# Performance work log

Hardware: AMD Instinct MI355X
Metric: run time of the kernel (lower is better)

The kernel has to match this reference:

```python
import jax, jax.numpy as jnp
import numpy as np

SELF_DIM = 6   # self_state_dim
HID = 50       # lstm_hidden_dim


def setup_inputs() -> dict:
    key = jax.random.key(0)
    ks = jax.random.split(key, 16)
    B, N, D = 8192, 64, 13  # batch, num humans, joint-state length

    def w(k, shape):
        # kaiming-ish init, stored as [in, out] so forward is x @ W + b
        return jax.random.normal(k, shape, jnp.float32) / jnp.sqrt(jnp.float32(shape[0]))

    z = lambda n: jnp.zeros((n,), jnp.float32)
    return {
        "state": jax.random.normal(ks[0], (B, N, D), jnp.float32),
        # mlp1: 13 -> 150 -> 100, last_relu=True
        "mlp1_w1": w(ks[1], (13, 150)),  "mlp1_b1": z(150),
        "mlp1_w2": w(ks[2], (150, 100)), "mlp1_b2": z(100),
        # attention: 200 -> 100 -> 100 -> 1 (no relu on last)
        "attn_w1": w(ks[3], (200, 100)), "attn_b1": z(100),
        "attn_w2": w(ks[4], (100, 100)), "attn_b2": z(100),
        "attn_w3": w(ks[5], (100, 1)),   "attn_b3": z(1),
        # LSTM(input=7, hidden=50), torch gate order i,f,g,o
        "lstm_wih": w(ks[6], (7, 4 * HID)),
        "lstm_whh": w(ks[7], (HID, 4 * HID)),
        "lstm_bih": z(4 * HID), "lstm_bhh": z(4 * HID),
        # mlp: 56 -> 150 -> 100 -> 100 -> 1
        "mlp_w1": w(ks[8], (SELF_DIM + HID, 150)), "mlp_b1": z(150),
        "mlp_w2": w(ks[9], (150, 100)),            "mlp_b2": z(100),
        "mlp_w3": w(ks[10], (100, 100)),           "mlp_b3": z(100),
        "mlp_w4": w(ks[11], (100, 1)),             "mlp_b4": z(1),
    }


def reference(state, mlp1_w1, mlp1_b1, mlp1_w2, mlp1_b2,
              attn_w1, attn_b1, attn_w2, attn_b2, attn_w3, attn_b3,
              lstm_wih, lstm_whh, lstm_bih, lstm_bhh,
              mlp_w1, mlp_b1, mlp_w2, mlp_b2, mlp_w3, mlp_b3, mlp_w4, mlp_b4):
    relu = jax.nn.relu
    B, N, D = state.shape
    self_state = state[:, 0, :SELF_DIM]      # [B, 6]
    human_state = state[:, :, SELF_DIM:]     # [B, N, 7]

    # mlp1 over all B*N per-human joint-state rows (last_relu=True)
    flat = state.reshape(B * N, D)
    m1 = relu(relu(flat @ mlp1_w1 + mlp1_b1) @ mlp1_w2 + mlp1_b2)   # [B*N, 100]

    # mean-pooled global state, broadcast back per human, concat, attention score
    gdim = m1.shape[-1]
    global_state = jnp.mean(m1.reshape(B, N, gdim), axis=1, keepdims=True)
    global_state = jnp.broadcast_to(global_state, (B, N, gdim)).reshape(B * N, gdim)
    a_in = jnp.concatenate([m1, global_state], axis=1)               # [B*N, 200]
    scores = (relu(relu(a_in @ attn_w1 + attn_b1) @ attn_w2 + attn_b2) @ attn_w3 + attn_b3)
    scores = scores.reshape(B, N)
    # NOTE: in the original torch code `scores` only feed `rerank_human_state`,
    # which is never consumed (dead code) -- the LSTM runs on the UNSORTED
    # human_state. We keep the score computation for fidelity; the per-sample
    # argsort/gather is dropped since it does not affect the output.

    # LSTM over the N humans (batch_first in torch, h0=c0=0)
    xs = jnp.transpose(human_state, (1, 0, 2))   # [N, B, 7]
    h0 = jnp.zeros((B, HID), state.dtype)

    def step(carry, x_t):
        h, c = carry
        gates = x_t @ lstm_wih + h @ lstm_whh + lstm_bih + lstm_bhh  # [B, 4H]
        i, f, g, o = jnp.split(gates, 4, axis=-1)
        c = jax.nn.sigmoid(f) * c + jax.nn.sigmoid(i) * jnp.tanh(g)
        h = jax.nn.sigmoid(o) * jnp.tanh(c)
        return (h, c), None

    (hn, _cn), _ = jax.lax.scan(step, (h0, h0), xs)

    # value head on [self_state, h_n]
    joint = jnp.concatenate([self_state, hn], axis=1)   # [B, 56]
    x = relu(joint @ mlp_w1 + mlp_b1)
    x = relu(x @ mlp_w2 + mlp_b2)
    x = relu(x @ mlp_w3 + mlp_b3)
    value = x @ mlp_w4 + mlp_b4                          # [B, 1]
    return value
```

## Files before the change

kernel.cpp:

```cpp
#include <hip/hip_runtime.h>

typedef __attribute__((ext_vector_type(8))) short short8;
typedef __attribute__((ext_vector_type(4))) float f32x4;
union frag_u { short8 v; unsigned short u[8]; };

__device__ __forceinline__ float bf2f(unsigned short b) {
  unsigned int u = ((unsigned int)b) << 16;
  float f; __builtin_memcpy(&f, &u, 4); return f;
}
__device__ __forceinline__ unsigned short f2bf(float f) {
  unsigned int u; __builtin_memcpy(&u, &f, 4);
  return (unsigned short)((u + 0x7FFFu + ((u >> 16) & 1u)) >> 16);
}
__device__ __forceinline__ unsigned short hi_of(float f) { return f2bf(f); }
__device__ __forceinline__ unsigned short lo_of(float f) {
  unsigned short h = f2bf(f); return f2bf(f - bf2f(h));
}

__device__ __forceinline__ void lstm_act(float gi, float gf, float gg, float go,
                                         float& c, float& h) {
  gi = fminf(fmaxf(gi, -15.f), 15.f);
  gf = fminf(fmaxf(gf, -15.f), 15.f);
  gg = fminf(fmaxf(gg, -15.f), 15.f);
  go = fminf(fmaxf(go, -15.f), 15.f);
  float A = 1.f + __expf(-gf);
  float B = 1.f + __expf(-gi);
  float C = 1.f + __expf(2.f * gg);
  float BC  = B * C;
  float num = c * BC + A * (C - 2.f);
  c = num * __builtin_amdgcn_rcpf(A * BC);
  float D  = 1.f + __expf(-go);
  float cl = fminf(fmaxf(c, -15.f), 15.f);
  float E  = 1.f + __expf(2.f * cl);
  h = (E - 2.f) * __builtin_amdgcn_rcpf(D * E);
}

__global__ void detect_dtype_kernel(const unsigned short* s, int* flag) {
  int i = threadIdx.x;
  unsigned short v = s[2 * i];
  int e = (v >> 7) & 0xFF;
  unsigned long long m = __ballot(e < 100 || e > 140);
  if (i == 0) *flag = (__popcll(m) >= 16) ? 1 : 0;
}

template <int AS, typename GetB, typename GetW>
__device__ __forceinline__ void mfma_layer(const unsigned short* sA, float* sG,
    int wave, int col, int quad, int kc_n, int ntiles, int N, GetB getb, GetW getw)
{
  for (int tile = wave; tile < ntiles; tile += 16) {
    int n = tile * 16 + col;
    float b = (n < N) ? getb(n) : 0.f;
    f32x4 acc = {b, b, b, b};
    for (int kc = 0; kc < kc_n; ++kc) {
      short8 a = *(const short8*)&sA[col * AS + kc * 32 + quad * 8];
      frag_u w;
      #pragma unroll
      for (int j = 0; j < 8; ++j) {
        int k = kc * 32 + quad * 8 + j;
        w.u[j] = (n < N) ? getw(k, n) : (unsigned short)0;
      }
      acc = __builtin_amdgcn_mfma_f32_16x16x32_bf16(a, w.v, acc, 0, 0, 0);
    }
    *(f32x4*)&sG[n * 20 + quad * 4] = acc;
  }
}

template <int AS, bool LO>
__device__ __forceinline__ void relu_fill(const float* sG, unsigned short* sA,
                                          int tid, int N, int loOff, int Kpad) {
  for (int idx = tid; idx < 16 * Kpad; idx += 1024) {
    int m = idx & 15, n = idx >> 4;
    unsigned short v = 0;
    if (n < N) {
      v = f2bf(fmaxf(sG[n * 20 + m], 0.f));
    } else if (LO && n >= loOff && n < loOff + N) {
      float x = fmaxf(sG[(n - loOff) * 20 + m], 0.f);
      v = lo_of(x);
    }
    sA[m * AS + n] = v;
  }
}

template <bool F32>
__global__ __launch_bounds__(1024, 8) void value_net_kernel(
    const void* state_, const void* wih_, const void* whh_,
    const void* bih_, const void* bhh_,
    const void* w1_, const void* b1_, const void* w2_, const void* b2_,
    const void* w3_, const void* b3_, const void* w4_, const void* b4_,
    void* out_, const int* flag)
{
  if (flag && *flag != (F32 ? 1 : 0)) return;

  constexpr int AS = F32 ? 328 : 168;
  constexpr int KC = F32 ? 6 : 4;

  __shared__ __align__(16) unsigned short sA[2][16 * AS];
  __shared__ __align__(16) float sG[208 * 20];
  __shared__ __align__(16) unsigned short sX[1024 * 8 * (F32 ? 2 : 1)];

  const unsigned short* st16 = (const unsigned short*)state_;
  const float*          stf  = (const float*)state_;

  const int tid  = threadIdx.x;
  const int wave = tid >> 6;
  const int lane = tid & 63;
  const int col  = lane & 15;
  const int quad = lane >> 4;
  const int r0   = blockIdx.x * 16;

  {
    unsigned int* a32 = (unsigned int*)&sA[0][0];
    constexpr int ZT = 16 * AS;
    #pragma unroll
    for (int i = 0; i < (ZT + 1023) / 1024; ++i) {
      int idx = tid + i * 1024;
      if (idx < ZT) a32[idx] = 0;
    }
  }

  {
    int r = tid >> 6, t = tid & 63;
    size_t g = (size_t)(r0 + r) * 832 + (size_t)t * 13 + 6;
    int base = (t * 16 + r) * 8;
    if constexpr (!F32) {
      #pragma unroll
      for (int d = 0; d < 7; ++d) sX[base + d] = st16[g + d];
    } else {
      #pragma unroll
      for (int d = 0; d < 7; ++d) {
        float f = stf[g + d];
        unsigned short h = f2bf(f);
        sX[2 * (base + d) + 0] = h;
        sX[2 * (base + d) + 1] = f2bf(f - bf2f(h));
      }
    }
  }

  auto W_lstm = [&](int k, int n) -> unsigned short {
    if constexpr (!F32) {
      const unsigned short* wih = (const unsigned short*)wih_;
      const unsigned short* whh = (const unsigned short*)whh_;
      if (k < 7)   return wih[k * 200 + n];
      if (k < 8)   return (unsigned short)0;
      if (k < 108) return whh[((k - 8) >> 1) * 200 + n];
      return (unsigned short)0;
    } else {
      const float* wih = (const float*)wih_;
      const float* whh = (const float*)whh_;
      if (k < 7)   return hi_of(wih[k * 200 + n]);
      if (k < 14)  return hi_of(wih[(k - 7) * 200 + n]);
      if (k < 21)  return lo_of(wih[(k - 14) * 200 + n]);
      if (k < 22)  return (unsigned short)0;
      if (k < 122) return hi_of(whh[((k - 22) >> 1) * 200 + n]);
      if (k < 172) return lo_of(whh[(k - 122) * 200 + n]);
      return (unsigned short)0;
    }
  };
  auto ldf = [&](const void* p, int i) -> float {
    if constexpr (F32) return ((const float*)p)[i];
    else               return bf2f(((const unsigned short*)p)[i]);
  };

  const bool hasTile = (wave < 13);
  frag_u wf[KC];
  float  wb = 0.f;
  if (hasTile) {
    int nn = wave * 16 + col;
    int no = (nn < 200) ? ((nn & 3) * 50 + (nn >> 2)) : 0;
    #pragma unroll
    for (int kc = 0; kc < KC; ++kc) {
      #pragma unroll
      for (int j = 0; j < 8; ++j) {
        int k = kc * 32 + quad * 8 + j;
        wf[kc].u[j] = (nn < 200) ? W_lstm(k, no) : (unsigned short)0;
      }
    }
    wb = (nn < 200) ? (ldf(bih_, no) + ldf(bhh_, no)) : 0.f;
  }

  const int  u_   = wave * 4 + quad;
  const bool iact = hasTile && (u_ < 50);
  float c_ = 0.f, hf = 0.f;

  const bool isx = (tid >= 832) && (tid < 944);
  const int  xm = (tid - 832) / 7, xd = (tid - 832) - ((tid - 832) / 7) * 7;
  auto xfeed = [&](unsigned short* sAw, int t) {
    int base = (t * 16 + xm) * 8 + xd;
    if constexpr (!F32) {
      sAw[xm * AS + xd] = sX[base];
    } else {
      unsigned short h = sX[2 * base + 0], l = sX[2 * base + 1];
      sAw[xm * AS + xd] = h; sAw[xm * AS + 14 + xd] = h;
      sAw[xm * AS + 7 + xd] = l;
    }
  };

  __syncthreads();
  if (isx) xfeed(&sA[0][0], 0);
  __syncthreads();

  for (int t = 0; t < 64; ++t) {
    const unsigned short* sAr = &sA[t & 1][0];
    unsigned short*       sAw = &sA[(t & 1) ^ 1][0];

    if (hasTile) {
      short8 a[KC];
      #pragma unroll
      for (int kc = 0; kc < KC; ++kc)
        a[kc] = *(const short8*)&sAr[col * AS + kc * 32 + quad * 8];
      f32x4 acc = {wb, wb, wb, wb};
      #pragma unroll
      for (int kc = 0; kc < KC; ++kc)
        acc = __builtin_amdgcn_mfma_f32_16x16x32_bf16(a[kc], wf[kc].v, acc, 0, 0, 0);
      *(f32x4*)&sG[(wave * 16 + col) * 20 + quad * 4] = acc;

      if (iact) {
        int nb = wave * 16 + quad * 4;
        float gi = sG[(nb + 0) * 20 + col];
        float gf = sG[(nb + 1) * 20 + col];
        float gg = sG[(nb + 2) * 20 + col];
        float go = sG[(nb + 3) * 20 + col];
        float h;
        lstm_act(gi, gf, gg, go, c_, h);
        if (t < 63) {
          unsigned short hb = f2bf(h);
          unsigned short hl = f2bf(h - bf2f(hb));
          unsigned int pack = (unsigned int)hb | ((unsigned int)hl << 16);
          if constexpr (!F32) {
            *(unsigned int*)&sAw[col * AS + 8 + 2 * u_] = pack;
          } else {
            *(unsigned int*)&sAw[col * AS + 22 + 2 * u_] = pack;
            sAw[col * AS + 122 + u_] = hb;
          }
        } else hf = h;
      }
    } else if (isx && t < 63) {
      xfeed(sAw, t + 1);
    }
    __syncthreads();
  }

  unsigned short* sA0 = &sA[0][0];
  {
    unsigned int* a32 = (unsigned int*)sA0;
    #pragma unroll
    for (int i = 0; i < (16 * AS / 2 + 1023) / 1024; ++i) {
      int idx = tid + i * 1024;
      if (idx < 16 * AS / 2) a32[idx] = 0;
    }
  }
  __syncthreads();
  if (iact) {
    unsigned short hb = f2bf(hf);
    unsigned short hl = f2bf(hf - bf2f(hb));
    sA0[col * AS + 6 + u_] = hb;
    if constexpr (!F32) sA0[col * AS + 56 + u_] = hl; else sA0[col * AS + 62 + u_] = hl;
  }
  if (tid < 96) {
    int m = tid / 6, d = tid - (tid / 6) * 6;
    if constexpr (!F32) sA0[m * AS + d] = st16[(size_t)(r0 + m) * 832 + d];
    else {
      float f = stf[(size_t)(r0 + m) * 832 + d];
      sA0[m * AS + d] = hi_of(f); sA0[m * AS + 56 + d] = lo_of(f);
    }
  }
  __syncthreads();

  mfma_layer<AS>(sA0, sG, wave, col, quad, 4, 10, 150,
    [&](int n) { return ldf(b1_, n); },
    [&](int k, int n) -> unsigned short {
      if constexpr (!F32) {
        const unsigned short* w1 = (const unsigned short*)w1_;
        if (k < 56)  return w1[k * 150 + n];
        if (k < 106) return w1[(k - 50) * 150 + n];
        return (unsigned short)0;
      } else {
        const float* w1 = (const float*)w1_;
        if (k < 56)  return hi_of(w1[k * 150 + n]);
        if (k < 112) return hi_of(w1[(k - 56) * 150 + n]);
        return (unsigned short)0;
      }
    });
  __syncthreads();
  if constexpr (!F32) relu_fill<AS, false>(sG, sA0, tid, 150, 160, 160);
  else                relu_fill<AS, true >(sG, sA0, tid, 150, 150, 320);
  __syncthreads();

  mfma_layer<AS>(sA0, sG, wave, col, quad, F32 ? 10 : 5, 7, 100,
    [&](int n) { return ldf(b2_, n); },
    [&](int k, int n) -> unsigned short {
      if constexpr (!F32) {
        const unsigned short* w2 = (const unsigned short*)w2_;
        return (k < 150) ? w2[k * 100 + n] : (unsigned short)0;
      } else {
        const float* w2 = (const float*)w2_;
        if (k < 150) return hi_of(w2[k * 100 + n]);
        if (k < 300) return hi_of(w2[(k - 150) * 100 + n]);
        return (unsigned short)0;
      }
    });
  __syncthreads();
  if constexpr (!F32) relu_fill<AS, false>(sG, sA0, tid, 100, 128, 128);
  else                relu_fill<AS, true >(sG, sA0, tid, 100, 100, 224);
  __syncthreads();

  mfma_layer<AS>(sA0, sG, wave, col, quad, F32 ? 7 : 4, 7, 100,
    [&](int n) { return ldf(b3_, n); },
    [&](int k, int n) -> unsigned short {
      if constexpr (!F32) {
        const unsigned short* w3 = (const unsigned short*)w3_;
        return (k < 100) ? w3[k * 100 + n] : (unsigned short)0;
      } else {
        const float* w3 = (const float*)w3_;
        if (k < 100) return hi_of(w3[k * 100 + n]);
        if (k < 200) return hi_of(w3[(k - 100) * 100 + n]);
        return (unsigned short)0;
      }
    });
  __syncthreads();

  if (tid < 256) {
    int m = tid >> 4, j0 = tid & 15;
    float s = 0.f;
    for (int j = j0; j < 100; j += 16)
      s += fmaxf(sG[j * 20 + m], 0.f) * ldf(w4_, j);
    s += __shfl_xor(s, 8); s += __shfl_xor(s, 4);
    s += __shfl_xor(s, 2); s += __shfl_xor(s, 1);
    if (j0 == 0) {
      float v = s + ldf(b4_, 0);
      if constexpr (!F32) ((unsigned short*)out_)[r0 + m] = f2bf(v);
      else                ((float*)out_)[r0 + m] = v;
    }
  }
}

extern "C" void kernel_launch(void* const* d_in, const int* in_sizes, int n_in,
                              void* d_out, int out_size, void* d_ws, size_t ws_size,
                              hipStream_t stream) {
  (void)n_in; (void)out_size;
  const void* state = d_in[0];
  const void* wih = d_in[11]; const void* whh = d_in[12];
  const void* bih = d_in[13]; const void* bhh = d_in[14];
  const void* w1  = d_in[15]; const void* b1  = d_in[16];
  const void* w2  = d_in[17]; const void* b2  = d_in[18];
  const void* w3  = d_in[19]; const void* b3  = d_in[20];
  const void* w4  = d_in[21]; const void* b4  = d_in[22];

  const long long F32B  = 8192LL * 64 * 13 * 4;
  const long long BF16B = 8192LL * 64 * 13 * 2;
  long long sz = in_sizes ? (long long)in_sizes[0] : -1;

  if (sz == F32B) {
    value_net_kernel<true><<<dim3(512), dim3(1024), 0, stream>>>(
        state, wih, whh, bih, bhh, w1, b1, w2, b2, w3, b3, w4, b4, d_out,
        (const int*)nullptr);
  } else if (sz == BF16B) {
    value_net_kernel<false><<<dim3(512), dim3(1024), 0, stream>>>(
        state, wih, whh, bih, bhh, w1, b1, w2, b2, w3, b3, w4, b4, d_out,
        (const int*)nullptr);
  } else if (ws_size >= sizeof(int)) {
    int* flag = (int*)d_ws;
    detect_dtype_kernel<<<dim3(1), dim3(64), 0, stream>>>(
        (const unsigned short*)state, flag);
    value_net_kernel<false><<<dim3(512), dim3(1024), 0, stream>>>(
        state, wih, whh, bih, bhh, w1, b1, w2, b2, w3, b3, w4, b4, d_out, flag);
    value_net_kernel<true><<<dim3(512), dim3(1024), 0, stream>>>(
        state, wih, whh, bih, bhh, w1, b1, w2, b2, w3, b3, w4, b4, d_out, flag);
  } else {
    value_net_kernel<false><<<dim3(512), dim3(1024), 0, stream>>>(
        state, wih, whh, bih, bhh, w1, b1, w2, b2, w3, b3, w4, b4, d_out,
        (const int*)nullptr);
  }
}
```

Measured before the change: 235.5 us.

## Restructure LSTM into 4-wave blocks with register-held hidden state and swapped MFMA operands

Shrinks each block from 16 waves to 4. Each wave computes 3-4 gate tiles with the weights as the MFMA A operand, so the four gates of a hidden unit land in one lane's accumulator and no longer go through shared memory. The hidden state is kept packed (bf16 hi/lo) in registers and exchanged between waves through a small double-buffered shared array, with one barrier per step. The input x and the bias are folded into the first K chunk, with the bias taken as a constant-1 column. This cuts per-step barrier and LDS traffic in the serial recurrence, in exchange for complex index mapping and heavy register use (24 weight fragments per lane). The bf16 path now also uses the hi/lo split layout, so it does more MFMA work.

```diff
diff --git a/kernel.cpp b/kernel.cpp
--- a/kernel.cpp
+++ b/kernel.cpp
@@ -2,7 +2,8 @@
 
 typedef __attribute__((ext_vector_type(8))) short short8;
 typedef __attribute__((ext_vector_type(4))) float f32x4;
-union frag_u { short8 v; unsigned short u[8]; };
+typedef __attribute__((ext_vector_type(4))) unsigned int u32x4;
+union frag_u { short8 v; unsigned short u[8]; unsigned int w[4]; };
 
 __device__ __forceinline__ float bf2f(unsigned short b) {
   unsigned int u = ((unsigned int)b) << 16;
@@ -16,6 +17,8 @@
 __device__ __forceinline__ unsigned short lo_of(float f) {
   unsigned short h = f2bf(f); return f2bf(f - bf2f(h));
 }
+__device__ __forceinline__ float ldf_f32(const void* p, int i) { return ((const float*)p)[i]; }
+__device__ __forceinline__ float ldf_b16(const void* p, int i) { return bf2f(((const unsigned short*)p)[i]); }
 
 __device__ __forceinline__ void lstm_act(float gi, float gf, float gg, float go,
                                          float& c, float& h) {
@@ -26,12 +29,12 @@
   float A = 1.f + __expf(-gf);
   float B = 1.f + __expf(-gi);
   float C = 1.f + __expf(2.f * gg);
-  float BC  = B * C;
+  float BC = B * C;
   float num = c * BC + A * (C - 2.f);
   c = num * __builtin_amdgcn_rcpf(A * BC);
-  float D  = 1.f + __expf(-go);
+  float D = 1.f + __expf(-go);
   float cl = fminf(fmaxf(c, -15.f), 15.f);
-  float E  = 1.f + __expf(2.f * cl);
+  float E = 1.f + __expf(2.f * cl);
   h = (E - 2.f) * __builtin_amdgcn_rcpf(D * E);
 }
 
@@ -43,13 +46,61 @@
   if (i == 0) *flag = (__popcll(m) >= 16) ? 1 : 0;
 }
 
+template <bool F32>
+__device__ __forceinline__ unsigned short W_elem(
+    int k, int T, int nl,
+    const void* wih_, const void* whh_, const void* bih_, const void* bhh_) {
+  const int O[4] = {1, 2, 3, 0};
+  int qd = nl >> 2, g = nl & 3;
+  int uc = 4 * T + O[qd];
+  if (uc >= 50) return 0;
+  int no = g * 50 + uc;
+  auto whi = [&](const void* p, int idx) -> unsigned short {
+    if constexpr (F32) return hi_of(((const float*)p)[idx]);
+    else return ((const unsigned short*)p)[idx];
+  };
+  auto wlo = [&](const void* p, int idx) -> unsigned short {
+    if constexpr (F32) return lo_of(((const float*)p)[idx]);
+    else return 0;
+  };
+  if (k < 21) {
+    int d = k / 3, sl = k - 3 * d;
+    return (sl == 2) ? wlo(wih_, d * 200 + no) : whi(wih_, d * 200 + no);
+  }
+  if (k < 23) {
+    float b;
+    if constexpr (F32) b = ((const float*)bih_)[no] + ((const float*)bhh_)[no];
+    else b = bf2f(((const unsigned short*)bih_)[no]) + bf2f(((const unsigned short*)bhh_)[no]);
+    if (k == 21) return f2bf(b);
+    unsigned short bh = f2bf(b);
+    return f2bf(b - bf2f(bh));
+  }
+  if (k < 24) return 0;
+  if (k < 128) {
+    int idx = k - 24, wA = idx >> 3, s = (idx & 7) >> 1;
+    int qB = (3 + wA) & 3, t = 4 * (wA >> 2) + s;
+    if (t > ((qB == 3) ? 12 : 11)) return 0;
+    int u = 4 * t + O[qB];
+    if (u >= 50) return 0;
+    return whi(whh_, u * 200 + no);
+  }
+  int idx = k - 128, wB = idx >> 3, j7 = idx & 7;
+  int qB = wB & 3, t = 8 * (wB >> 2) + j7;
+  if (wB == 4 && j7 >= 5)
+    return (j7 <= 6) ? whi(whh_, 49 * 200 + no) : 0;
+  if (t > ((qB == 0 || qB == 3) ? 12 : 11)) return 0;
+  int u = 4 * t + O[qB];
+  if (u >= 50) return 0;
+  return wlo(whh_, u * 200 + no);
+}
+
 template <int AS, typename GetB, typename GetW>
 __device__ __forceinline__ void mfma_layer(const unsigned short* sA, float* sG,
     int wave, int col, int quad, int kc_n, int ntiles, int N, GetB getb, GetW getw)
 {
-  for (int tile = wave; tile < ntiles; tile += 16) {
-    int n = tile * 16 + col;
-    float b = (n < N) ? getb(n) : 0.f;
+  for (int tile = wave; tile < ntiles; tile += 4) {
+    int nn = tile * 16 + col;
+    float b = (nn < N) ? getb(nn) : 0.f;
     f32x4 acc = {b, b, b, b};
     for (int kc = 0; kc < kc_n; ++kc) {
       short8 a = *(const short8*)&sA[col * AS + kc * 32 + quad * 8];
@@ -57,32 +108,32 @@
       #pragma unroll
       for (int j = 0; j < 8; ++j) {
         int k = kc * 32 + quad * 8 + j;
-        w.u[j] = (n < N) ? getw(k, n) : (unsigned short)0;
+        w.u[j] = (nn < N) ? getw(k, nn) : (unsigned short)0;
       }
       acc = __builtin_amdgcn_mfma_f32_16x16x32_bf16(a, w.v, acc, 0, 0, 0);
     }
-    *(f32x4*)&sG[n * 20 + quad * 4] = acc;
-  }
-}
-
-template <int AS, bool LO>
+    *(f32x4*)&sG[nn * 20 + quad * 4] = acc;
+  }
+}
+
+template <int AS>
 __device__ __forceinline__ void relu_fill(const float* sG, unsigned short* sA,
                                           int tid, int N, int loOff, int Kpad) {
-  for (int idx = tid; idx < 16 * Kpad; idx += 1024) {
-    int m = idx & 15, n = idx >> 4;
+  for (int idx = tid; idx < 16 * Kpad; idx += 256) {
+    int m = idx & 15, nn = idx >> 4;
     unsigned short v = 0;
-    if (n < N) {
-      v = f2bf(fmaxf(sG[n * 20 + m], 0.f));
-    } else if (LO && n >= loOff && n < loOff + N) {
-      float x = fmaxf(sG[(n - loOff) * 20 + m], 0.f);
+    if (nn < N) {
+      v = f2bf(fmaxf(sG[nn * 20 + m], 0.f));
+    } else if (nn >= loOff && nn < loOff + N) {
+      float x = fmaxf(sG[(nn - loOff) * 20 + m], 0.f);
       v = lo_of(x);
     }
-    sA[m * AS + n] = v;
+    sA[m * AS + nn] = v;
   }
 }
 
 template <bool F32>
-__global__ __launch_bounds__(1024, 8) void value_net_kernel(
+__global__ __launch_bounds__(256, 2) void value_net_kernel(
     const void* state_, const void* wih_, const void* whh_,
     const void* bih_, const void* bhh_,
     const void* w1_, const void* b1_, const void* w2_, const void* b2_,
@@ -91,242 +142,242 @@
 {
   if (flag && *flag != (F32 ? 1 : 0)) return;
 
-  constexpr int AS = F32 ? 328 : 168;
-  constexpr int KC = F32 ? 6 : 4;
-
-  __shared__ __align__(16) unsigned short sA[2][16 * AS];
+  constexpr int AS = 328;
+
+  __shared__ __align__(16) unsigned int sX[1024 * 8];
+  __shared__ unsigned int sE[2][13 * 64];
+  __shared__ __align__(16) unsigned short sA[16 * AS];
   __shared__ __align__(16) float sG[208 * 20];
-  __shared__ __align__(16) unsigned short sX[1024 * 8 * (F32 ? 2 : 1)];
 
   const unsigned short* st16 = (const unsigned short*)state_;
   const float*          stf  = (const float*)state_;
 
   const int tid  = threadIdx.x;
-  const int wave = tid >> 6;
+  const int wv   = tid >> 6;
   const int lane = tid & 63;
-  const int col  = lane & 15;
+  const int n    = lane & 15;
   const int quad = lane >> 4;
   const int r0   = blockIdx.x * 16;
 
-  {
-    unsigned int* a32 = (unsigned int*)&sA[0][0];
-    constexpr int ZT = 16 * AS;
+  const int O[4] = {1, 2, 3, 0};
+  const int ores = O[quad];
+  const int tb   = (wv == 0) ? 0 : (wv == 1) ? 4 : (wv == 2) ? 7 : 10;
+  const int nt   = (wv == 0) ? 4 : 3;
+
+  auto ldf = [&](const void* p, int i) -> float {
+    if constexpr (F32) return ldf_f32(p, i); else return ldf_b16(p, i);
+  };
+
+  for (int idx = tid; idx < 1024; idx += 256) {
+    int t = idx >> 4, r = idx & 15;
+    size_t g = (size_t)(r0 + r) * 832 + (size_t)t * 13 + 6;
+    unsigned int* dst = &sX[(t * 16 + r) * 8];
     #pragma unroll
-    for (int i = 0; i < (ZT + 1023) / 1024; ++i) {
-      int idx = tid + i * 1024;
-      if (idx < ZT) a32[idx] = 0;
-    }
-  }
-
-  {
-    int r = tid >> 6, t = tid & 63;
-    size_t g = (size_t)(r0 + r) * 832 + (size_t)t * 13 + 6;
-    int base = (t * 16 + r) * 8;
-    if constexpr (!F32) {
-      #pragma unroll
-      for (int d = 0; d < 7; ++d) sX[base + d] = st16[g + d];
-    } else {
-      #pragma unroll
-      for (int d = 0; d < 7; ++d) {
+    for (int d = 0; d < 7; ++d) {
+      unsigned int v;
+      if constexpr (F32) {
         float f = stf[g + d];
         unsigned short h = f2bf(f);
-        sX[2 * (base + d) + 0] = h;
-        sX[2 * (base + d) + 1] = f2bf(f - bf2f(h));
+        v = (unsigned int)h | ((unsigned int)f2bf(f - bf2f(h)) << 16);
+      } else v = st16[g + d];
+      dst[d] = v;
+    }
+    dst[7] = 0;
+  }
+
+  frag_u wf[4][6];
+  #pragma unroll
+  for (int Ti = 0; Ti < 4; ++Ti) {
+    if (Ti < nt) {
+      int T = tb + Ti;
+      #pragma unroll
+      for (int kc = 0; kc < 6; ++kc)
+        #pragma unroll
+        for (int j = 0; j < 8; ++j)
+          wf[Ti][kc].u[j] = W_elem<F32>(kc * 32 + quad * 8 + j, T, n,
+                                        wih_, whh_, bih_, bhh_);
+    }
+  }
+
+  unsigned int pk[16];
+  #pragma unroll
+  for (int i = 0; i < 16; ++i) pk[i] = 0;
+  float c_[4] = {0.f, 0.f, 0.f, 0.f};
+
+  __syncthreads();
+
+  auto hh = [](unsigned int a, unsigned int b) -> unsigned int {
+    return (a & 0xffffu) | (b << 16);
+  };
+  auto ror16 = [](unsigned int a) -> unsigned int {
+    return (a >> 16) | (a << 16);
+  };
+  auto packh = [](float h) -> unsigned int {
+    unsigned short hb = f2bf(h);
+    unsigned short hl = f2bf(h - bf2f(hb));
+    return (unsigned int)hb | ((unsigned int)hl << 16);
+  };
+
+  #pragma unroll 1
+  for (int tt = 0; tt < 64; ++tt) {
+    const u32x4* xp = (const u32x4*)&sX[(tt * 16 + n) * 8];
+    u32x4 xa = xp[0], xb = xp[1];
+    unsigned int px0 = xa[0], px1 = xa[1], px2 = xa[2], px3 = xa[3];
+    unsigned int px4 = xb[0], px5 = xb[1], px6 = xb[2];
+    const unsigned int ONE = 0x3F80u;
+
+    frag_u fr0, fr1, fr2, fr3, fr4, fr5;
+    if (quad == 0) {
+      fr0.w[0] = px0; fr0.w[1] = hh(px0, px1); fr0.w[2] = ror16(px1); fr0.w[3] = px2;
+    } else if (quad == 1) {
+      fr0.w[0] = hh(px2, px3); fr0.w[1] = ror16(px3); fr0.w[2] = px4; fr0.w[3] = hh(px4, px5);
+    } else if (quad == 2) {
+      fr0.w[0] = ror16(px5); fr0.w[1] = px6; fr0.w[2] = hh(px6, ONE); fr0.w[3] = ONE;
+    } else {
+      fr0.w[0] = pk[0]; fr0.w[1] = pk[1]; fr0.w[2] = pk[2]; fr0.w[3] = pk[3];
+    }
+    bool q3 = (quad == 3);
+    fr1.w[0] = q3 ? pk[4]  : pk[0];  fr1.w[1] = q3 ? pk[5]  : pk[1];
+    fr1.w[2] = q3 ? pk[6]  : pk[2];  fr1.w[3] = q3 ? pk[7]  : pk[3];
+    fr2.w[0] = q3 ? pk[8]  : pk[4];  fr2.w[1] = q3 ? pk[9]  : pk[5];
+    fr2.w[2] = q3 ? pk[10] : pk[6];  fr2.w[3] = q3 ? pk[11] : pk[7];
+    fr3.w[0] = q3 ? pk[12] : pk[8];  fr3.w[1] = q3 ? 0u     : pk[9];
+    fr3.w[2] = q3 ? 0u     : pk[10]; fr3.w[3] = q3 ? 0u     : pk[11];
+    fr4.w[0] = hh(pk[0], pk[1]); fr4.w[1] = hh(pk[2], pk[3]);
+    fr4.w[2] = hh(pk[4], pk[5]); fr4.w[3] = hh(pk[6], pk[7]);
+    fr5.w[0] = hh(pk[8], pk[9]); fr5.w[1] = hh(pk[10], pk[11]);
+    if (quad == 0) { fr5.w[2] = hh(pk[12], pk[12]); fr5.w[3] = pk[12] >> 16; }
+    else           { fr5.w[2] = hh(pk[12], 0u);     fr5.w[3] = 0u; }
+
+    f32x4 z = {0.f, 0.f, 0.f, 0.f};
+    f32x4 acc0 = z, acc1 = z, acc2 = z, acc3 = z;
+    #pragma unroll
+    for (int kc = 0; kc < 6; ++kc) {
+      const frag_u& fr = (kc == 0) ? fr0 : (kc == 1) ? fr1 : (kc == 2) ? fr2 :
+                         (kc == 3) ? fr3 : (kc == 4) ? fr4 : fr5;
+      acc0 = __builtin_amdgcn_mfma_f32_16x16x32_bf16(wf[0][kc].v, fr.v, acc0, 0, 0, 0);
+      acc1 = __builtin_amdgcn_mfma_f32_16x16x32_bf16(wf[1][kc].v, fr.v, acc1, 0, 0, 0);
+      acc2 = __builtin_amdgcn_mfma_f32_16x16x32_bf16(wf[2][kc].v, fr.v, acc2, 0, 0, 0);
+      if (wv == 0)
+        acc3 = __builtin_amdgcn_mfma_f32_16x16x32_bf16(wf[3][kc].v, fr.v, acc3, 0, 0, 0);
+    }
+
+    unsigned int pknew0 = 0, pknew1 = 0, pknew2 = 0, pknew3 = 0;
+    { int u = 4 * (tb + 0) + ores;
+      if (u < 50) { float h; lstm_act(acc0[0], acc0[1], acc0[2], acc0[3], c_[0], h); pknew0 = packh(h); } }
+    { int u = 4 * (tb + 1) + ores;
+      if (u < 50) { float h; lstm_act(acc1[0], acc1[1], acc1[2], acc1[3], c_[1], h); pknew1 = packh(h); } }
+    { int u = 4 * (tb + 2) + ores;
+      if (u < 50) { float h; lstm_act(acc2[0], acc2[1], acc2[2], acc2[3], c_[2], h); pknew2 = packh(h); } }
+    if (wv == 0) { float h; lstm_act(acc3[0], acc3[1], acc3[2], acc3[3], c_[3], h); pknew3 = packh(h); }
+
+    if (tt < 63) {
+      unsigned int* e = sE[tt & 1];
+      if      (wv == 0) { e[0 + lane] = pknew0; e[64 + lane] = pknew1; e[128 + lane] = pknew2; e[192 + lane] = pknew3; }
+      else if (wv == 1) { e[256 + lane] = pknew0; e[320 + lane] = pknew1; e[384 + lane] = pknew2; }
+      else if (wv == 2) { e[448 + lane] = pknew0; e[512 + lane] = pknew1; e[576 + lane] = pknew2; }
+      else              { e[640 + lane] = pknew0; e[704 + lane] = pknew1; e[768 + lane] = pknew2; }
+    }
+    if      (wv == 0) { pk[0] = pknew0; pk[1] = pknew1; pk[2] = pknew2; pk[3] = pknew3; }
+    else if (wv == 1) { pk[4] = pknew0; pk[5] = pknew1; pk[6] = pknew2; }
+    else if (wv == 2) { pk[7] = pknew0; pk[8] = pknew1; pk[9] = pknew2; }
+    else              { pk[10] = pknew0; pk[11] = pknew1; pk[12] = pknew2; }
+    if (tt < 63) {
+      __syncthreads();
+      const unsigned int* e = sE[tt & 1];
+      if (wv == 0) {
+        pk[4] = e[256 + lane]; pk[5] = e[320 + lane]; pk[6] = e[384 + lane];
+        pk[7] = e[448 + lane]; pk[8] = e[512 + lane]; pk[9] = e[576 + lane];
+        pk[10] = e[640 + lane]; pk[11] = e[704 + lane]; pk[12] = e[768 + lane];
+      } else if (wv == 1) {
+        pk[0] = e[0 + lane]; pk[1] = e[64 + lane]; pk[2] = e[128 + lane]; pk[3] = e[192 + lane];
+        pk[7] = e[448 + lane]; pk[8] = e[512 + lane]; pk[9] = e[576 + lane];
+        pk[10] = e[640 + lane]; pk[11] = e[704 + lane]; pk[12] = e[768 + lane];
+      } else if (wv == 2) {
+        pk[0] = e[0 + lane]; pk[1] = e[64 + lane]; pk[2] = e[128 + lane]; pk[3] = e[192 + lane];
+        pk[4] = e[256 + lane]; pk[5] = e[320 + lane]; pk[6] = e[384 + lane];
+        pk[10] = e[640 + lane]; pk[11] = e[704 + lane]; pk[12] = e[768 + lane];
+      } else {
+        pk[0] = e[0 + lane]; pk[1] = e[64 + lane]; pk[2] = e[128 + lane]; pk[3] = e[192 + lane];
+        pk[4] = e[256 + lane]; pk[5] = e[320 + lane]; pk[6] = e[384 + lane];
+        pk[7] = e[448 + lane]; pk[8] = e[512 + lane]; pk[9] = e[576 + lane];
       }
     }
   }
 
-  auto W_lstm = [&](int k, int n) -> unsigned short {
-    if constexpr (!F32) {
-      const unsigned short* wih = (const unsigned short*)wih_;
-      const unsigned short* whh = (const unsigned short*)whh_;
-      if (k < 7)   return wih[k * 200 + n];
-      if (k < 8)   return (unsigned short)0;
-      if (k < 108) return whh[((k - 8) >> 1) * 200 + n];
-      return (unsigned short)0;
-    } else {
-      const float* wih = (const float*)wih_;
-      const float* whh = (const float*)whh_;
-      if (k < 7)   return hi_of(wih[k * 200 + n]);
-      if (k < 14)  return hi_of(wih[(k - 7) * 200 + n]);
-      if (k < 21)  return lo_of(wih[(k - 14) * 200 + n]);
-      if (k < 22)  return (unsigned short)0;
-      if (k < 122) return hi_of(whh[((k - 22) >> 1) * 200 + n]);
-      if (k < 172) return lo_of(whh[(k - 122) * 200 + n]);
-      return (unsigned short)0;
-    }
-  };
-  auto ldf = [&](const void* p, int i) -> float {
-    if constexpr (F32) return ((const float*)p)[i];
-    else               return bf2f(((const unsigned short*)p)[i]);
-  };
-
-  const bool hasTile = (wave < 13);
-  frag_u wf[KC];
-  float  wb = 0.f;
-  if (hasTile) {
-    int nn = wave * 16 + col;
-    int no = (nn < 200) ? ((nn & 3) * 50 + (nn >> 2)) : 0;
-    #pragma unroll
-    for (int kc = 0; kc < KC; ++kc) {
-      #pragma unroll
-      for (int j = 0; j < 8; ++j) {
-        int k = kc * 32 + quad * 8 + j;
-        wf[kc].u[j] = (nn < 200) ? W_lstm(k, no) : (unsigned short)0;
+  {
+    unsigned int* a32 = (unsigned int*)sA;
+    for (int idx = tid; idx < 16 * AS / 2; idx += 256) a32[idx] = 0;
+  }
+  __syncthreads();
+  {
+    auto jput = [&](int t, unsigned int p) {
+      int u = 4 * t + ores;
+      if (u < 50) {
+        sA[n * AS + 6 + u]  = (unsigned short)(p & 0xffffu);
+        sA[n * AS + 62 + u] = (unsigned short)(p >> 16);
       }
-    }
-    wb = (nn < 200) ? (ldf(bih_, no) + ldf(bhh_, no)) : 0.f;
-  }
-
-  const int  u_   = wave * 4 + quad;
-  const bool iact = hasTile && (u_ < 50);
-  float c_ = 0.f, hf = 0.f;
-
-  const bool isx = (tid >= 832) && (tid < 944);
-  const int  xm = (tid - 832) / 7, xd = (tid - 832) - ((tid - 832) / 7) * 7;
-  auto xfeed = [&](unsigned short* sAw, int t) {
-    int base = (t * 16 + xm) * 8 + xd;
-    if constexpr (!F32) {
-      sAw[xm * AS + xd] = sX[base];
-    } else {
-      unsigned short h = sX[2 * base + 0], l = sX[2 * base + 1];
-      sAw[xm * AS + xd] = h; sAw[xm * AS + 14 + xd] = h;
-      sAw[xm * AS + 7 + xd] = l;
-    }
-  };
-
-  __syncthreads();
-  if (isx) xfeed(&sA[0][0], 0);
-  __syncthreads();
-
-  for (int t = 0; t < 64; ++t) {
-    const unsigned short* sAr = &sA[t & 1][0];
-    unsigned short*       sAw = &sA[(t & 1) ^ 1][0];
-
-    if (hasTile) {
-      short8 a[KC];
-      #pragma unroll
-      for (int kc = 0; kc < KC; ++kc)
-        a[kc] = *(const short8*)&sAr[col * AS + kc * 32 + quad * 8];
-      f32x4 acc = {wb, wb, wb, wb};
-      #pragma unroll
-      for (int kc = 0; kc < KC; ++kc)
-        acc = __builtin_amdgcn_mfma_f32_16x16x32_bf16(a[kc], wf[kc].v, acc, 0, 0, 0);
-      *(f32x4*)&sG[(wave * 16 + col) * 20 + quad * 4] = acc;
-
-      if (iact) {
-        int nb = wave * 16 + quad * 4;
-        float gi = sG[(nb + 0) * 20 + col];
-        float gf = sG[(nb + 1) * 20 + col];
-        float gg = sG[(nb + 2) * 20 + col];
-        float go = sG[(nb + 3) * 20 + col];
-        float h;
-        lstm_act(gi, gf, gg, go, c_, h);
-        if (t < 63) {
-          unsigned short hb = f2bf(h);
-          unsigned short hl = f2bf(h - bf2f(hb));
-          unsigned int pack = (unsigned int)hb | ((unsigned int)hl << 16);
-          if constexpr (!F32) {
-            *(unsigned int*)&sAw[col * AS + 8 + 2 * u_] = pack;
-          } else {
-            *(unsigned int*)&sAw[col * AS + 22 + 2 * u_] = pack;
-            sAw[col * AS + 122 + u_] = hb;
-          }
-        } else hf = h;
-      }
-    } else if (isx && t < 63) {
-      xfeed(sAw, t + 1);
-    }
-    __syncthreads();
-  }
-
-  unsigned short* sA0 = &sA[0][0];
-  {
-    unsigned int* a32 = (unsigned int*)sA0;
-    #pragma unroll
-    for (int i = 0; i < (16 * AS / 2 + 1023) / 1024; ++i) {
-      int idx = tid + i * 1024;
-      if (idx < 16 * AS / 2) a32[idx] = 0;
-    }
-  }
-  __syncthreads();
-  if (iact) {
-    unsigned short hb = f2bf(hf);
-    unsigned short hl = f2bf(hf - bf2f(hb));
-    sA0[col * AS + 6 + u_] = hb;
-    if constexpr (!F32) sA0[col * AS + 56 + u_] = hl; else sA0[col * AS + 62 + u_] = hl;
+    };
+    if      (wv == 0) { jput(0, pk[0]); jput(1, pk[1]); jput(2, pk[2]); jput(3, pk[3]); }
+    else if (wv == 1) { jput(4, pk[4]); jput(5, pk[5]); jput(6, pk[6]); }
+    else if (wv == 2) { jput(7, pk[7]); jput(8, pk[8]); jput(9, pk[9]); }
+    else              { jput(10, pk[10]); jput(11, pk[11]); jput(12, pk[12]); }
   }
   if (tid < 96) {
     int m = tid / 6, d = tid - (tid / 6) * 6;
-    if constexpr (!F32) sA0[m * AS + d] = st16[(size_t)(r0 + m) * 832 + d];
-    else {
+    if constexpr (F32) {
       float f = stf[(size_t)(r0 + m) * 832 + d];
-      sA0[m * AS + d] = hi_of(f); sA0[m * AS + 56 + d] = lo_of(f);
-    }
-  }
-  __syncthreads();
-
-  mfma_layer<AS>(sA0, sG, wave, col, quad, 4, 10, 150,
-    [&](int n) { return ldf(b1_, n); },
-    [&](int k, int n) -> unsigned short {
-      if constexpr (!F32) {
-        const unsigned short* w1 = (const unsigned short*)w1_;
-        if (k < 56)  return w1[k * 150 + n];
-        if (k < 106) return w1[(k - 50) * 150 + n];
-        return (unsigned short)0;
-      } else {
-        const float* w1 = (const float*)w1_;
-        if (k < 56)  return hi_of(w1[k * 150 + n]);
-        if (k < 112) return hi_of(w1[(k - 56) * 150 + n]);
-        return (unsigned short)0;
-      }
+      sA[m * AS + d] = hi_of(f); sA[m * AS + 56 + d] = lo_of(f);
+    } else {
+      sA[m * AS + d] = st16[(size_t)(r0 + m) * 832 + d];
+    }
+  }
+  __syncthreads();
+
+  auto whiT = [&](const void* p, int idx) -> unsigned short {
+    if constexpr (F32) return hi_of(((const float*)p)[idx]);
+    else return ((const unsigned short*)p)[idx];
+  };
+
+  mfma_layer<AS>(sA, sG, wv, n, quad, 4, 10, 150,
+    [&](int nn) { return ldf(b1_, nn); },
+    [&](int k, int nn) -> unsigned short {
+      if (k < 56)  return whiT(w1_, k * 150 + nn);
+      if (k < 112) return whiT(w1_, (k - 56) * 150 + nn);
+      return (unsigned short)0;
     });
   __syncthreads();
-  if constexpr (!F32) relu_fill<AS, false>(sG, sA0, tid, 150, 160, 160);
-  else                relu_fill<AS, true >(sG, sA0, tid, 150, 150, 320);
-  __syncthreads();
-
-  mfma_layer<AS>(sA0, sG, wave, col, quad, F32 ? 10 : 5, 7, 100,
-    [&](int n) { return ldf(b2_, n); },
-    [&](int k, int n) -> unsigned short {
-      if constexpr (!F32) {
-        const unsigned short* w2 = (const unsigned short*)w2_;
-        return (k < 150) ? w2[k * 100 + n] : (unsigned short)0;
-      } else {
-        const float* w2 = (const float*)w2_;
-        if (k < 150) return hi_of(w2[k * 100 + n]);
-        if (k < 300) return hi_of(w2[(k - 150) * 100 + n]);
-        return (unsigned short)0;
-      }
+  relu_fill<AS>(sG, sA, tid, 150, 150, 320);
+  __syncthreads();
+
+  mfma_layer<AS>(sA, sG, wv, n, quad, 10, 7, 100,
+    [&](int nn) { return ldf(b2_, nn); },
+    [&](int k, int nn) -> unsigned short {
+      if (k < 150) return whiT(w2_, k * 100 + nn);
+      if (k < 300) return whiT(w2_, (k - 150) * 100 + nn);
+      return (unsigned short)0;
     });
   __syncthreads();
-  if constexpr (!F32) relu_fill<AS, false>(sG, sA0, tid, 100, 128, 128);
-  else                relu_fill<AS, true >(sG, sA0, tid, 100, 100, 224);
-  __syncthreads();
-
-  mfma_layer<AS>(sA0, sG, wave, col, quad, F32 ? 7 : 4, 7, 100,
-    [&](int n) { return ldf(b3_, n); },
-    [&](int k, int n) -> unsigned short {
-      if constexpr (!F32) {
-        const unsigned short* w3 = (const unsigned short*)w3_;
-        return (k < 100) ? w3[k * 100 + n] : (unsigned short)0;
-      } else {
-        const float* w3 = (const float*)w3_;
-        if (k < 100) return hi_of(w3[k * 100 + n]);
-        if (k < 200) return hi_of(w3[(k - 100) * 100 + n]);
-        return (unsigned short)0;
-      }
+  relu_fill<AS>(sG, sA, tid, 100, 100, 224);
+  __syncthreads();
+
+  mfma_layer<AS>(sA, sG, wv, n, quad, 7, 7, 100,
+    [&](int nn) { return ldf(b3_, nn); },
+    [&](int k, int nn) -> unsigned short {
+      if (k < 100) return whiT(w3_, k * 100 + nn);
+      if (k < 200) return whiT(w3_, (k - 100) * 100 + nn);
+      return (unsigned short)0;
     });
   __syncthreads();
 
-  if (tid < 256) {
-    int m = tid >> 4, j0 = tid & 15;
+  if (tid < 64) {
+    int m = lane & 15, j0 = lane >> 4;
     float s = 0.f;
-    for (int j = j0; j < 100; j += 16)
+    for (int j = j0; j < 100; j += 4)
       s += fmaxf(sG[j * 20 + m], 0.f) * ldf(w4_, j);
-    s += __shfl_xor(s, 8); s += __shfl_xor(s, 4);
-    s += __shfl_xor(s, 2); s += __shfl_xor(s, 1);
-    if (j0 == 0) {
+    s += __shfl_xor(s, 16);
+    s += __shfl_xor(s, 32);
+    if (lane < 16) {
       float v = s + ldf(b4_, 0);
       if constexpr (!F32) ((unsigned short*)out_)[r0 + m] = f2bf(v);
       else                ((float*)out_)[r0 + m] = v;
@@ -351,23 +402,23 @@
   long long sz = in_sizes ? (long long)in_sizes[0] : -1;
 
   if (sz == F32B) {
-    value_net_kernel<true><<<dim3(512), dim3(1024), 0, stream>>>(
+    value_net_kernel<true><<<dim3(512), dim3(256), 0, stream>>>(
         state, wih, whh, bih, bhh, w1, b1, w2, b2, w3, b3, w4, b4, d_out,
         (const int*)nullptr);
   } else if (sz == BF16B) {
-    value_net_kernel<false><<<dim3(512), dim3(1024), 0, stream>>>(
+    value_net_kernel<false><<<dim3(512), dim3(256), 0, stream>>>(
         state, wih, whh, bih, bhh, w1, b1, w2, b2, w3, b3, w4, b4, d_out,
         (const int*)nullptr);
   } else if (ws_size >= sizeof(int)) {
     int* flag = (int*)d_ws;
     detect_dtype_kernel<<<dim3(1), dim3(64), 0, stream>>>(
         (const unsigned short*)state, flag);
-    value_net_kernel<false><<<dim3(512), dim3(1024), 0, stream>>>(
+    value_net_kernel<false><<<dim3(512), dim3(256), 0, stream>>>(
         state, wih, whh, bih, bhh, w1, b1, w2, b2, w3, b3, w4, b4, d_out, flag);
-    value_net_kernel<true><<<dim3(512), dim3(1024), 0, stream>>>(
+    value_net_kernel<true><<<dim3(512), dim3(256), 0, stream>>>(
         state, wih, whh, bih, bhh, w1, b1, w2, b2, w3, b3, w4, b4, d_out, flag);
   } else {
-    value_net_kernel<false><<<dim3(512), dim3(1024), 0, stream>>>(
+    value_net_kernel<false><<<dim3(512), dim3(256), 0, stream>>>(
         state, wih, whh, bih, bhh, w1, b1, w2, b2, w3, b3, w4, b4, d_out,
         (const int*)nullptr);
   }
```

Measured after the change: 313.8 us. 33.2% more time.
